# Performance work log

Measured on AMD Instinct MI355X. Metric: run time of the kernel, lower is better.

Reference implementation:

```python
import jax, jax.numpy as jnp
import numpy as np


def _log_g(x):
    # log of g(x) = where(x>=0, x+0.5, sigmoid(x)), computed stably in log space
    return jnp.where(x >= 0.0, jnp.log(jax.nn.relu(x) + 0.5), -jax.nn.softplus(-x))


def setup_inputs() -> dict:
    key = jax.random.key(0)
    k1, k2, k3, k4 = jax.random.split(key, 4)
    B, T, D, H = 4, 8192, 512, 512
    x = jax.random.normal(k1, (B, T, D), dtype=jnp.float32)
    h_prev = jax.random.uniform(k2, (B, 1, H), dtype=jnp.float32)  # positive: log(h0) taken
    W_h = jax.random.normal(k3, (H, D), dtype=jnp.float32) * (1.0 / np.sqrt(D))
    b_h = jnp.zeros((H,), dtype=jnp.float32)
    W_z = jax.random.normal(k4, (H, D), dtype=jnp.float32) * (1.0 / np.sqrt(D))
    b_z = jnp.zeros((H,), dtype=jnp.float32)
    return {"x": x, "h_prev": h_prev, "W_h": W_h, "b_h": b_h, "W_z": W_z, "b_z": b_z}


def reference(x, h_prev, W_h, b_h, W_z, b_z):
    # parallel (seq_len > 1) minGRU forward via Heinsen log-space scan
    k = jnp.einsum('btd,hd->bth', x, W_z) + b_z           # (B,T,H) gate pre-activation
    log_z = -jax.nn.softplus(-k)                          # log sigmoid(k)
    log_coeffs = -jax.nn.softplus(k)                      # log (1 - sigmoid(k))
    log_tilde_h = _log_g(jnp.einsum('btd,hd->bth', x, W_h) + b_h)
    log_h0 = jnp.log(h_prev)                              # (B,1,H)
    log_values = jnp.concatenate([log_h0, log_z + log_tilde_h], axis=1)  # (B,T+1,H)
    # a_star = [0, cumsum(log_coeffs)]
    a_star = jnp.pad(jnp.cumsum(log_coeffs, axis=1), ((0, 0), (1, 0), (0, 0)))
    log_h = a_star + jax.lax.cumlogsumexp(log_values - a_star, axis=1)
    h = jnp.exp(log_h)[:, 1:]                             # drop h0 -> (B,T,H)
    return h
```

## Files before the change

### kernel.cpp

```cpp
#include <hip/hip_runtime.h>
#include <hip/hip_bf16.h>
#include <stdint.h>

#define B_ 4
#define T_ 8192
#define D_ 512
#define H_ 512
#define M_ (B_ * T_)
#define SEG 32
#define SPB 256
#define NSEG (M_ / SEG)

typedef __attribute__((ext_vector_type(8))) short short8;
typedef __attribute__((ext_vector_type(4))) float floatx4;
typedef __attribute__((ext_vector_type(2))) float float2e;

__device__ __forceinline__ unsigned short f2bf(float f) {
    union { float f; unsigned int u; } v; v.f = f;
    unsigned int u = v.u;
    u += 0x7fffu + ((u >> 16) & 1u);
    return (unsigned short)(u >> 16);
}
__device__ __forceinline__ float bf_lo(unsigned int u) {
    union { unsigned int i; float f; } a; a.i = u << 16; return a.f;
}
__device__ __forceinline__ float bf_hi(unsigned int u) {
    union { unsigned int i; float f; } a; a.i = u & 0xffff0000u; return a.f;
}
__device__ __forceinline__ unsigned int pk_cd(float c, float d) {
    return (unsigned int)f2bf(c) | ((unsigned int)f2bf(d) << 16);
}

__global__ void conv_all(const float* __restrict__ x,
                         const float* __restrict__ Wz,
                         const float* __restrict__ Wh,
                         unsigned short* __restrict__ xbf,
                         unsigned short* __restrict__ Wf)
{
    const int X4 = M_ * D_ / 4;
    const int W4 = H_ * D_ / 4;
    int i = blockIdx.x * blockDim.x + threadIdx.x;
    const float* src; unsigned short* dst; int idx;
    if (i < X4)             { src = x;  dst = xbf;                  idx = i; }
    else if (i < X4 + W4)   { src = Wz; dst = Wf;                   idx = i - X4; }
    else if (i < X4 + 2*W4) { src = Wh; dst = Wf + (size_t)H_ * D_; idx = i - X4 - W4; }
    else return;
    float4 v = ((const float4*)src)[idx];
    ushort4 w; w.x = f2bf(v.x); w.y = f2bf(v.y); w.z = f2bf(v.z); w.w = f2bf(v.w);
    ((ushort4*)dst)[idx] = w;
}

#define LDSB 35840

__global__ __launch_bounds__(256, 4)
void gemm_cd(const unsigned short* __restrict__ xbf,
             const unsigned short* __restrict__ Wf,
             const float* __restrict__ bz, const float* __restrict__ bh,
             unsigned int* __restrict__ cd,
             float2* __restrict__ Sagg)
{
    __shared__ __align__(16) char smem[LDSB];
    unsigned short* lds = (unsigned short*)smem;
    unsigned int*   cdl = (unsigned int*)smem;

    const int tid  = threadIdx.x;
    const int lane = tid & 63;
    const int wave = tid >> 6;
    const int xcd  = blockIdx.x & 7;
    const int nblk = (blockIdx.x >> 3) & 7;
    const int mblk = xcd * 32 + (blockIdx.x >> 6);
    const int m0 = mblk * 128;
    const int n0 = nblk * 64;
    const int wm = (wave >> 1) * 64;
    const int wn = (wave & 1) * 32;
    const int l15  = lane & 15;
    const int quad = lane >> 4;
    const int srow = lane >> 2;
    const int sp   = lane & 3;

    #define STAGE(p, kt)                                                          \
    {                                                                             \
        const int kb = (kt) * 32;                                                 \
        unsigned short* bb = lds + (p) * 8192;                                    \
        _Pragma("unroll")                                                         \
        for (int r = 0; r < 2; ++r) {                                             \
            const int chunk = r * 4 + wave;                                       \
            const int row   = chunk * 16 + srow;                                  \
            const int kp    = sp ^ (row & 3);                                     \
            __builtin_amdgcn_global_load_lds(                                     \
                (const __attribute__((address_space(1))) unsigned int*)           \
                    (xbf + (size_t)(m0 + row) * D_ + kb + kp * 8),                \
                (__attribute__((address_space(3))) unsigned int*)(bb + chunk * 512),\
                16, 0, 0);                                                        \
        }                                                                         \
        {                                                                         \
            const int row = wave * 16 + srow;                                     \
            const int kp  = sp ^ (row & 3);                                       \
            __builtin_amdgcn_global_load_lds(                                     \
                (const __attribute__((address_space(1))) unsigned int*)           \
                    (Wf + (size_t)(n0 + row) * D_ + kb + kp * 8),                 \
                (__attribute__((address_space(3))) unsigned int*)(bb + 4096 + wave * 512),\
                16, 0, 0);                                                        \
            __builtin_amdgcn_global_load_lds(                                     \
                (const __attribute__((address_space(1))) unsigned int*)           \
                    (Wf + (size_t)(512 + n0 + row) * D_ + kb + kp * 8),           \
                (__attribute__((address_space(3))) unsigned int*)(bb + 6144 + wave * 512),\
                16, 0, 0);                                                        \
        }                                                                         \
    }

    floatx4 acc_z[4][2], acc_h[4][2];
    #pragma unroll
    for (int i = 0; i < 4; ++i)
        #pragma unroll
        for (int j = 0; j < 2; ++j) { acc_z[i][j] = (floatx4)0.0f; acc_h[i][j] = (floatx4)0.0f; }

    STAGE(0, 0);

    for (int kt = 0; kt < 16; ++kt) {
        __syncthreads();
        const int base = (kt & 1) * 8192;
        short8 af[4], zf[2], hf[2];
        #pragma unroll
        for (int i = 0; i < 4; ++i) {
            const int ra = wm + i * 16 + l15;
            af[i] = *(const short8*)&lds[base + ra * 32 + ((quad ^ (ra & 3)) * 8)];
        }
        #pragma unroll
        for (int j = 0; j < 2; ++j) {
            const int rb = wn + j * 16 + l15;
            zf[j] = *(const short8*)&lds[base + 4096 + rb * 32 + ((quad ^ (rb & 3)) * 8)];
            hf[j] = *(const short8*)&lds[base + 6144 + rb * 32 + ((quad ^ (rb & 3)) * 8)];
        }
        if (kt < 15) STAGE((kt + 1) & 1, kt + 1);
        #pragma unroll
        for (int i = 0; i < 4; ++i)
            #pragma unroll
            for (int j = 0; j < 2; ++j) {
                acc_z[i][j] = __builtin_amdgcn_mfma_f32_16x16x32_bf16(zf[j], af[i], acc_z[i][j], 0, 0, 0);
                acc_h[i][j] = __builtin_amdgcn_mfma_f32_16x16x32_bf16(hf[j], af[i], acc_h[i][j], 0, 0, 0);
            }
    }

    __syncthreads();

    #pragma unroll
    for (int j = 0; j < 2; ++j) {
        const int hlb = wn + j * 16 + quad * 4;
        const float4 bzv = *(const float4*)&bz[n0 + hlb];
        const float4 bhv = *(const float4*)&bh[n0 + hlb];
        #pragma unroll
        for (int i = 0; i < 4; ++i) {
            const int mloc = wm + i * 16 + l15;
            uint4 w;
            #pragma unroll
            for (int r = 0; r < 4; ++r) {
                float kz = acc_z[i][j][r] + ((const float*)&bzv)[r];
                float hp = acc_h[i][j][r] + ((const float*)&bhv)[r];
                float c  = 1.0f / (1.0f + __expf(kz));
                float g  = (hp >= 0.0f) ? (hp + 0.5f) : (1.0f / (1.0f + __expf(-hp)));
                float d  = (1.0f - c) * g;
                ((unsigned int*)&w)[r] = pk_cd(c, d);
            }
            *(uint4*)&cd[(size_t)(m0 + mloc) * H_ + n0 + hlb] = w;
            *(uint4*)&cdl[mloc * 68 + hlb] = w;
        }
    }

    __syncthreads();

    {
        float C = 1.0f, Dv = 0.0f;
        const int t0 = wave * 32;
        #pragma unroll
        for (int t = 0; t < 32; ++t) {
            unsigned int u = cdl[(t0 + t) * 68 + lane];
            float c = bf_lo(u), d = bf_hi(u);
            Dv = fmaf(c, Dv, d);
            C *= c;
        }
        const int chain = (m0 >> 13) * 512 + n0 + lane;
        const int seg   = ((m0 >> 5) & 255) + wave;
        Sagg[(size_t)chain * SPB + seg] = make_float2(C, Dv);
    }
    #undef STAGE
}

__global__ __launch_bounds__(256)
void interseg(const float* __restrict__ h_prev,
              const float2* __restrict__ Sagg,
              float* __restrict__ Hseg)
{
    const int chain = blockIdx.x * 4 + (threadIdx.x >> 6);
    const int lane  = threadIdx.x & 63;
    const float2* spp = Sagg + (size_t)chain * SPB + lane * 4;
    float4 q0 = *(const float4*)&spp[0];
    float4 q1 = *(const float4*)&spp[2];
    float C = q0.x, D = q0.y;
    D = fmaf(q0.z, D, q0.w);  C *= q0.z;
    D = fmaf(q1.x, D, q1.y);  C *= q1.x;
    D = fmaf(q1.z, D, q1.w);  C *= q1.z;
    #pragma unroll
    for (int off = 1; off < 64; off <<= 1) {
        float Cp = __shfl_up(C, off, 64);
        float Dp = __shfl_up(D, off, 64);
        if (lane >= off) { D = fmaf(C, Dp, D); C *= Cp; }
    }
    float Ce = __shfl_up(C, 1, 64);
    float De = __shfl_up(D, 1, 64);
    if (lane == 0) { Ce = 1.0f; De = 0.0f; }
    const float h0 = h_prev[chain];
    float hs = fmaf(Ce, h0, De);
    float4 o;
    o.x = hs;
    hs = fmaf(q0.x, hs, q0.y); o.y = hs;
    hs = fmaf(q0.z, hs, q0.w); o.z = hs;
    hs = fmaf(q1.x, hs, q1.y); o.w = hs;
    *(float4*)&Hseg[(size_t)chain * SPB + lane * 4] = o;
}

__global__ __launch_bounds__(256)
void apply_scan(const unsigned int* __restrict__ cd,
                const float* __restrict__ Hseg,
                float* __restrict__ out)
{
    const int sg = blockIdx.x;
    const int b  = sg >> 8;
    const int s  = sg & 255;
    const int h  = threadIdx.x * 2;
    float hs0 = Hseg[(size_t)(b * 512 + h)     * SPB + s];
    float hs1 = Hseg[(size_t)(b * 512 + h + 1) * SPB + s];
    const unsigned int* base = cd + (size_t)sg * SEG * H_ + h;
    float* ob = out + (size_t)sg * SEG * H_ + h;
    uint2 v = *(const uint2*)base;
    #pragma unroll
    for (int t = 0; t < SEG; ++t) {
        uint2 vn;
        if (t < SEG - 1) vn = *(const uint2*)(base + (size_t)(t + 1) * H_);
        hs0 = fmaf(bf_lo(v.x), hs0, bf_hi(v.x));
        hs1 = fmaf(bf_lo(v.y), hs1, bf_hi(v.y));
        float2e o; o.x = hs0; o.y = hs1;
        __builtin_nontemporal_store(o, (float2e*)(ob + (size_t)t * H_));
        v = vn;
    }
}

extern "C" void kernel_launch(void* const* d_in, const int* in_sizes, int n_in,
                              void* d_out, int out_size, void* d_ws, size_t ws_size,
                              hipStream_t stream)
{
    const float* x      = (const float*)d_in[0];
    const float* h_prev = (const float*)d_in[1];
    const float* W_h    = (const float*)d_in[2];
    const float* b_h    = (const float*)d_in[3];
    const float* W_z    = (const float*)d_in[4];
    const float* b_z    = (const float*)d_in[5];
    float* out = (float*)d_out;

    unsigned short* xbf = (unsigned short*)d_out;

    char* ws = (char*)d_ws;
    unsigned int* cd = (unsigned int*)ws;
    size_t cd_bytes = (size_t)M_ * H_ * 4;
    unsigned short* Wf = (unsigned short*)(ws + cd_bytes);
    size_t wf_bytes = (size_t)2 * H_ * D_ * sizeof(unsigned short);
    float2* Sagg = (float2*)(ws + cd_bytes + wf_bytes);
    float*  Hseg = (float*)((char*)Sagg + (size_t)2048 * SPB * sizeof(float2));

    {
        int total = M_ * D_ / 4 + 2 * (H_ * D_ / 4);
        conv_all<<<dim3((total + 255) / 256), dim3(256), 0, stream>>>(x, W_z, W_h, xbf, Wf);
    }
    gemm_cd<<<dim3((M_ / 128) * (H_ / 64)), dim3(256), 0, stream>>>(
        xbf, Wf, b_z, b_h, cd, Sagg);
    interseg<<<dim3(512), dim3(256), 0, stream>>>(h_prev, Sagg, Hseg);
    apply_scan<<<dim3(NSEG), dim3(256), 0, stream>>>(cd, Hseg, out);
}
```

Baseline: 197.7 us.

## Vectorize conversion kernel, swizzle LDS cd tile, batch loads in apply scan

The conversion kernel now uses a grid-stride loop with 8-element nontemporal loads and 16-byte bf16 stores, running on a fixed 2048-block grid instead of one thread per float4. The GEMM epilogue's LDS staging of packed c/d values drops the padded 68-word row stride for a 64-word stride with an XOR swizzle, which shrinks LDS use and aims to keep bank conflicts down. apply_scan now issues all 32 row loads up front before the sequential recurrence, so more memory requests are in flight at once. The cost is more registers in apply_scan, which could lower occupancy.

New measurement: 197.9 us. No clear change (+0.1%).

```diff
diff --git a/kernel.cpp b/kernel.cpp
--- a/kernel.cpp
+++ b/kernel.cpp
@@ -31,26 +31,44 @@
     return (unsigned int)f2bf(c) | ((unsigned int)f2bf(d) << 16);
 }
 
-__global__ void conv_all(const float* __restrict__ x,
-                         const float* __restrict__ Wz,
-                         const float* __restrict__ Wh,
-                         unsigned short* __restrict__ xbf,
-                         unsigned short* __restrict__ Wf)
-{
-    const int X4 = M_ * D_ / 4;
-    const int W4 = H_ * D_ / 4;
-    int i = blockIdx.x * blockDim.x + threadIdx.x;
-    const float* src; unsigned short* dst; int idx;
-    if (i < X4)             { src = x;  dst = xbf;                  idx = i; }
-    else if (i < X4 + W4)   { src = Wz; dst = Wf;                   idx = i - X4; }
-    else if (i < X4 + 2*W4) { src = Wh; dst = Wf + (size_t)H_ * D_; idx = i - X4 - W4; }
-    else return;
-    float4 v = ((const float4*)src)[idx];
-    ushort4 w; w.x = f2bf(v.x); w.y = f2bf(v.y); w.z = f2bf(v.z); w.w = f2bf(v.w);
-    ((ushort4*)dst)[idx] = w;
-}
-
-#define LDSB 35840
+#define X8 (M_ * D_ / 8)
+#define W8 (H_ * D_ / 8)
+
+__global__ __launch_bounds__(256)
+void conv_all(const float* __restrict__ x,
+              const float* __restrict__ Wz,
+              const float* __restrict__ Wh,
+              unsigned short* __restrict__ xbf,
+              unsigned short* __restrict__ Wf)
+{
+    const int gid    = blockIdx.x * blockDim.x + threadIdx.x;
+    const int stride = gridDim.x * blockDim.x;
+    for (int i = gid; i < X8; i += stride) {
+        floatx4 a = __builtin_nontemporal_load((const floatx4*)x + 2 * i);
+        floatx4 b = __builtin_nontemporal_load((const floatx4*)x + 2 * i + 1);
+        short8 w;
+        w[0] = (short)f2bf(a[0]); w[1] = (short)f2bf(a[1]);
+        w[2] = (short)f2bf(a[2]); w[3] = (short)f2bf(a[3]);
+        w[4] = (short)f2bf(b[0]); w[5] = (short)f2bf(b[1]);
+        w[6] = (short)f2bf(b[2]); w[7] = (short)f2bf(b[3]);
+        *((short8*)xbf + i) = w;
+    }
+    if (gid < 2 * W8) {
+        const int i = gid;
+        const float* src = (i < W8) ? Wz : Wh;
+        const int idx = (i < W8) ? i : i - W8;
+        floatx4 a = __builtin_nontemporal_load((const floatx4*)src + 2 * idx);
+        floatx4 b = __builtin_nontemporal_load((const floatx4*)src + 2 * idx + 1);
+        short8 w;
+        w[0] = (short)f2bf(a[0]); w[1] = (short)f2bf(a[1]);
+        w[2] = (short)f2bf(a[2]); w[3] = (short)f2bf(a[3]);
+        w[4] = (short)f2bf(b[0]); w[5] = (short)f2bf(b[1]);
+        w[6] = (short)f2bf(b[2]); w[7] = (short)f2bf(b[3]);
+        *((short8*)Wf + i) = w;
+    }
+}
+
+#define LDSB 32768
 
 __global__ __launch_bounds__(256, 4)
 void gemm_cd(const unsigned short* __restrict__ xbf,
@@ -163,7 +181,7 @@
                 ((unsigned int*)&w)[r] = pk_cd(c, d);
             }
             *(uint4*)&cd[(size_t)(m0 + mloc) * H_ + n0 + hlb] = w;
-            *(uint4*)&cdl[mloc * 68 + hlb] = w;
+            *(uint4*)&cdl[mloc * 64 + (hlb ^ ((mloc & 7) << 2))] = w;
         }
     }
 
@@ -174,7 +192,8 @@
         const int t0 = wave * 32;
         #pragma unroll
         for (int t = 0; t < 32; ++t) {
-            unsigned int u = cdl[(t0 + t) * 68 + lane];
+            const int row = t0 + t;
+            unsigned int u = cdl[row * 64 + (lane ^ ((row & 7) << 2))];
             float c = bf_lo(u), d = bf_hi(u);
             Dv = fmaf(c, Dv, d);
             C *= c;
@@ -228,20 +247,20 @@
     const int b  = sg >> 8;
     const int s  = sg & 255;
     const int h  = threadIdx.x * 2;
+    const unsigned int* base = cd + (size_t)sg * SEG * H_ + h;
+    float* ob = out + (size_t)sg * SEG * H_ + h;
+    uint2 v[SEG];
+    #pragma unroll
+    for (int t = 0; t < SEG; ++t)
+        v[t] = *(const uint2*)(base + (size_t)t * H_);
     float hs0 = Hseg[(size_t)(b * 512 + h)     * SPB + s];
     float hs1 = Hseg[(size_t)(b * 512 + h + 1) * SPB + s];
-    const unsigned int* base = cd + (size_t)sg * SEG * H_ + h;
-    float* ob = out + (size_t)sg * SEG * H_ + h;
-    uint2 v = *(const uint2*)base;
     #pragma unroll
     for (int t = 0; t < SEG; ++t) {
-        uint2 vn;
-        if (t < SEG - 1) vn = *(const uint2*)(base + (size_t)(t + 1) * H_);
-        hs0 = fmaf(bf_lo(v.x), hs0, bf_hi(v.x));
-        hs1 = fmaf(bf_lo(v.y), hs1, bf_hi(v.y));
+        hs0 = fmaf(bf_lo(v[t].x), hs0, bf_hi(v[t].x));
+        hs1 = fmaf(bf_lo(v[t].y), hs1, bf_hi(v[t].y));
         float2e o; o.x = hs0; o.y = hs1;
         __builtin_nontemporal_store(o, (float2e*)(ob + (size_t)t * H_));
-        v = vn;
     }
 }
 
@@ -267,10 +286,7 @@
     float2* Sagg = (float2*)(ws + cd_bytes + wf_bytes);
     float*  Hseg = (float*)((char*)Sagg + (size_t)2048 * SPB * sizeof(float2));
 
-    {
-        int total = M_ * D_ / 4 + 2 * (H_ * D_ / 4);
-        conv_all<<<dim3((total + 255) / 256), dim3(256), 0, stream>>>(x, W_z, W_h, xbf, Wf);
-    }
+    conv_all<<<dim3(2048), dim3(256), 0, stream>>>(x, W_z, W_h, xbf, Wf);
     gemm_cd<<<dim3((M_ / 128) * (H_ / 64)), dim3(256), 0, stream>>>(
         xbf, Wf, b_z, b_h, cd, Sagg);
     interseg<<<dim3(512), dim3(256), 0, stream>>>(h_prev, Sagg, Hseg);
```
